# Performance work log

Hardware: AMD Instinct MI355X
Metric: run time of the kernel (lower is better)

## Reference

```python
import jax, jax.numpy as jnp
import numpy as np

N_NODES = 100000
N_EDGES = 1000000
DIM = 64


def setup_inputs() -> dict:
    key = jax.random.key(0)
    k1, k2, k3, k4 = jax.random.split(key, 4)
    node_emb = jax.random.normal(k1, (N_NODES, DIM), dtype=jnp.float32)
    rel_emb = jax.random.normal(k2, (N_EDGES, DIM), dtype=jnp.float32)
    src = jax.random.randint(k3, (N_EDGES,), 0, N_NODES, dtype=jnp.int64)
    dst = jax.random.randint(k4, (N_EDGES,), 0, N_NODES, dtype=jnp.int64)
    return {"node_emb": node_emb, "rel_emb": rel_emb, "src": src, "dst": dst}


def reference(node_emb, rel_emb, src, dst):
    # DistMult edge score: sum_d head[e,d] * rel[e,d] * tail[e,d]
    head = node_emb[src]          # (E, D) gather
    tail = node_emb[dst]          # (E, D) gather
    score = jnp.sum(head * rel_emb * tail, axis=-1)  # (E,)
    return score
```

## Files before the change

### kernel.cpp

```cpp
#include <hip/hip_runtime.h>
#include <hip/hip_bf16.h>


#define DIM 64
#define LANES_PER_EDGE 16

typedef __attribute__((ext_vector_type(4))) float  float4n;
typedef __attribute__((ext_vector_type(4))) unsigned short ushort4n;

__device__ __forceinline__ float bf2f(unsigned short u) {
    unsigned int x = ((unsigned int)u) << 16;
    return __builtin_bit_cast(float, x);
}

__device__ __forceinline__ unsigned short f2bf_rne(float f) {
    unsigned int x = __builtin_bit_cast(unsigned int, f);
    unsigned int lsb = (x >> 16) & 1u;
    x += 0x7fffu + lsb;
    return (unsigned short)(x >> 16);
}

__global__ __launch_bounds__(256) void convert_nodes_kernel(
    const float* __restrict__ node_emb,
    unsigned short* __restrict__ node_bf,
    int n_elems4)
{
    int i = blockIdx.x * blockDim.x + threadIdx.x;
    const int stride = gridDim.x * blockDim.x;
    for (; i < n_elems4; i += stride) {
        const float4n v = *reinterpret_cast<const float4n*>(node_emb + (size_t)i * 4);
        ushort4n o;
        o.x = f2bf_rne(v.x);
        o.y = f2bf_rne(v.y);
        o.z = f2bf_rne(v.z);
        o.w = f2bf_rne(v.w);
        *reinterpret_cast<ushort4n*>(node_bf + (size_t)i * 4) = o;
    }
}

__global__ __launch_bounds__(256) void distmult_score_bf16_kernel(
    const unsigned short* __restrict__ node_bf,
    const float* __restrict__ rel_emb,
    const int* __restrict__ src,
    const int* __restrict__ dst,
    float* __restrict__ out,
    int n_edges)
{
    const int tid   = blockIdx.x * blockDim.x + threadIdx.x;
    const int lane  = tid & (LANES_PER_EDGE - 1);
    const int group = tid >> 4;
    const int n_groups = (gridDim.x * blockDim.x) >> 4;
    const int off = lane * 4;

    for (int e = group; e < n_edges; e += 2 * n_groups) {
        const int e2 = e + n_groups;
        const bool has2 = (e2 < n_edges);

        const int s1 = src[e];
        const int d1 = dst[e];
        const int s2 = has2 ? src[e2] : 0;
        const int d2 = has2 ? dst[e2] : 0;

        const float4n  r1 = *reinterpret_cast<const float4n*>(rel_emb + (size_t)e * DIM + off);
        const ushort4n h1 = *reinterpret_cast<const ushort4n*>(node_bf + (size_t)s1 * DIM + off);
        const ushort4n t1 = *reinterpret_cast<const ushort4n*>(node_bf + (size_t)d1 * DIM + off);

        float4n  r2 = {0,0,0,0};
        ushort4n h2 = {0,0,0,0}, t2 = {0,0,0,0};
        if (has2) {
            r2 = *reinterpret_cast<const float4n*>(rel_emb + (size_t)e2 * DIM + off);
            h2 = *reinterpret_cast<const ushort4n*>(node_bf + (size_t)s2 * DIM + off);
            t2 = *reinterpret_cast<const ushort4n*>(node_bf + (size_t)d2 * DIM + off);
        }

        float p1 = bf2f(h1.x) * r1.x * bf2f(t1.x)
                 + bf2f(h1.y) * r1.y * bf2f(t1.y)
                 + bf2f(h1.z) * r1.z * bf2f(t1.z)
                 + bf2f(h1.w) * r1.w * bf2f(t1.w);

        p1 += __shfl_xor(p1, 1, 64);
        p1 += __shfl_xor(p1, 2, 64);
        p1 += __shfl_xor(p1, 4, 64);
        p1 += __shfl_xor(p1, 8, 64);
        if (lane == 0) out[e] = p1;

        if (has2) {
            float p2 = bf2f(h2.x) * r2.x * bf2f(t2.x)
                     + bf2f(h2.y) * r2.y * bf2f(t2.y)
                     + bf2f(h2.z) * r2.z * bf2f(t2.z)
                     + bf2f(h2.w) * r2.w * bf2f(t2.w);

            p2 += __shfl_xor(p2, 1, 64);
            p2 += __shfl_xor(p2, 2, 64);
            p2 += __shfl_xor(p2, 4, 64);
            p2 += __shfl_xor(p2, 8, 64);
            if (lane == 0) out[e2] = p2;
        }
    }
}

__global__ __launch_bounds__(256) void distmult_score_f32_kernel(
    const float* __restrict__ node_emb,
    const float* __restrict__ rel_emb,
    const int* __restrict__ src,
    const int* __restrict__ dst,
    float* __restrict__ out,
    int n_edges)
{
    const int tid   = blockIdx.x * blockDim.x + threadIdx.x;
    const int lane  = tid & (LANES_PER_EDGE - 1);
    const int group = tid >> 4;
    const int n_groups = (gridDim.x * blockDim.x) >> 4;
    const int off = lane * 4;

    for (int e = group; e < n_edges; e += n_groups) {
        const int s = src[e];
        const int d = dst[e];
        const float4n r = *reinterpret_cast<const float4n*>(rel_emb  + (size_t)e * DIM + off);
        const float4n h = *reinterpret_cast<const float4n*>(node_emb + (size_t)s * DIM + off);
        const float4n t = *reinterpret_cast<const float4n*>(node_emb + (size_t)d * DIM + off);

        float p = h.x * r.x * t.x + h.y * r.y * t.y + h.z * r.z * t.z + h.w * r.w * t.w;
        p += __shfl_xor(p, 1, 64);
        p += __shfl_xor(p, 2, 64);
        p += __shfl_xor(p, 4, 64);
        p += __shfl_xor(p, 8, 64);
        if (lane == 0) out[e] = p;
    }
}

extern "C" void kernel_launch(void* const* d_in, const int* in_sizes, int n_in,
                              void* d_out, int out_size, void* d_ws, size_t ws_size,
                              hipStream_t stream) {
    const float* node_emb = (const float*)d_in[0];
    const float* rel_emb  = (const float*)d_in[1];
    const int*   src      = (const int*)d_in[2];
    const int*   dst      = (const int*)d_in[3];
    float*       out      = (float*)d_out;

    const int n_edges     = in_sizes[2];
    const int n_node_elems = in_sizes[0];
    const size_t bf_bytes = (size_t)n_node_elems * sizeof(unsigned short);

    const int block = 256;
    long long blocks_needed = ((long long)n_edges * LANES_PER_EDGE + block - 1) / block;
    int grid = (int)(blocks_needed < 2048 ? blocks_needed : 2048);

    if (ws_size >= bf_bytes) {
        unsigned short* node_bf = (unsigned short*)d_ws;
        const int n4 = n_node_elems / 4;
        int cgrid = (n4 + block - 1) / block;
        if (cgrid > 2048) cgrid = 2048;
        convert_nodes_kernel<<<cgrid, block, 0, stream>>>(node_emb, node_bf, n4);
        distmult_score_bf16_kernel<<<grid, block, 0, stream>>>(node_bf, rel_emb, src, dst, out, n_edges);
    } else {
        distmult_score_f32_kernel<<<grid, block, 0, stream>>>(node_emb, rel_emb, src, dst, out, n_edges);
    }
}
```

Before: 85.84 us.

## Split scoring into two half-dimension passes to shrink gather working set

Splits the bf16 scoring kernel into two passes, each covering half of the embedding dimension. The intent is to halve the gathered node-table footprint per pass so it fits better in cache. The second pass reads back and accumulates into the output, and index and rel loads now use nontemporal hints. The cost is reading the src/dst indices twice, an extra output read-modify-write, and one more kernel launch.

```diff
diff --git a/kernel.cpp b/kernel.cpp
--- a/kernel.cpp
+++ b/kernel.cpp
@@ -3,7 +3,8 @@
 
 
 #define DIM 64
-#define LANES_PER_EDGE 16
+#define HALF_DIM 32
+#define LANES_PER_EDGE 8
 
 typedef __attribute__((ext_vector_type(4))) float  float4n;
 typedef __attribute__((ext_vector_type(4))) unsigned short ushort4n;
@@ -38,7 +39,8 @@
     }
 }
 
-__global__ __launch_bounds__(256) void distmult_score_bf16_kernel(
+template <int PASS>
+__global__ __launch_bounds__(256) void distmult_score_half_kernel(
     const unsigned short* __restrict__ node_bf,
     const float* __restrict__ rel_emb,
     const int* __restrict__ src,
@@ -48,53 +50,35 @@
 {
     const int tid   = blockIdx.x * blockDim.x + threadIdx.x;
     const int lane  = tid & (LANES_PER_EDGE - 1);
-    const int group = tid >> 4;
-    const int n_groups = (gridDim.x * blockDim.x) >> 4;
-    const int off = lane * 4;
+    const int group = tid >> 3;
+    const int n_groups = (gridDim.x * blockDim.x) >> 3;
+    const int off = PASS * HALF_DIM + lane * 4;
 
-    for (int e = group; e < n_edges; e += 2 * n_groups) {
-        const int e2 = e + n_groups;
-        const bool has2 = (e2 < n_edges);
+    for (int e = group; e < n_edges; e += n_groups) {
+        const int s = __builtin_nontemporal_load(src + e);
+        const int d = __builtin_nontemporal_load(dst + e);
 
-        const int s1 = src[e];
-        const int d1 = dst[e];
-        const int s2 = has2 ? src[e2] : 0;
-        const int d2 = has2 ? dst[e2] : 0;
+        const float4n  r = __builtin_nontemporal_load(
+            reinterpret_cast<const float4n*>(rel_emb + (size_t)e * DIM + off));
+        const ushort4n h = *reinterpret_cast<const ushort4n*>(node_bf + (size_t)s * DIM + off);
+        const ushort4n t = *reinterpret_cast<const ushort4n*>(node_bf + (size_t)d * DIM + off);
 
-        const float4n  r1 = *reinterpret_cast<const float4n*>(rel_emb + (size_t)e * DIM + off);
-        const ushort4n h1 = *reinterpret_cast<const ushort4n*>(node_bf + (size_t)s1 * DIM + off);
-        const ushort4n t1 = *reinterpret_cast<const ushort4n*>(node_bf + (size_t)d1 * DIM + off);
+        float p = bf2f(h.x) * r.x * bf2f(t.x)
+                + bf2f(h.y) * r.y * bf2f(t.y)
+                + bf2f(h.z) * r.z * bf2f(t.z)
+                + bf2f(h.w) * r.w * bf2f(t.w);
 
-        float4n  r2 = {0,0,0,0};
-        ushort4n h2 = {0,0,0,0}, t2 = {0,0,0,0};
-        if (has2) {
-            r2 = *reinterpret_cast<const float4n*>(rel_emb + (size_t)e2 * DIM + off);
-            h2 = *reinterpret_cast<const ushort4n*>(node_bf + (size_t)s2 * DIM + off);
-            t2 = *reinterpret_cast<const ushort4n*>(node_bf + (size_t)d2 * DIM + off);
-        }
+        p += __shfl_xor(p, 1, 64);
+        p += __shfl_xor(p, 2, 64);
+        p += __shfl_xor(p, 4, 64);
 
-        float p1 = bf2f(h1.x) * r1.x * bf2f(t1.x)
-                 + bf2f(h1.y) * r1.y * bf2f(t1.y)
-                 + bf2f(h1.z) * r1.z * bf2f(t1.z)
-                 + bf2f(h1.w) * r1.w * bf2f(t1.w);
-
-        p1 += __shfl_xor(p1, 1, 64);
-        p1 += __shfl_xor(p1, 2, 64);
-        p1 += __shfl_xor(p1, 4, 64);
-        p1 += __shfl_xor(p1, 8, 64);
-        if (lane == 0) out[e] = p1;
-
-        if (has2) {
-            float p2 = bf2f(h2.x) * r2.x * bf2f(t2.x)
-                     + bf2f(h2.y) * r2.y * bf2f(t2.y)
-                     + bf2f(h2.z) * r2.z * bf2f(t2.z)
-                     + bf2f(h2.w) * r2.w * bf2f(t2.w);
-
-            p2 += __shfl_xor(p2, 1, 64);
-            p2 += __shfl_xor(p2, 2, 64);
-            p2 += __shfl_xor(p2, 4, 64);
-            p2 += __shfl_xor(p2, 8, 64);
-            if (lane == 0) out[e2] = p2;
+        if (lane == 0) {
+            if (PASS == 0) {
+                __builtin_nontemporal_store(p, out + e);
+            } else {
+                const float prev = out[e];
+                __builtin_nontemporal_store(prev + p, out + e);
+            }
         }
     }
 }
@@ -108,7 +92,7 @@
     int n_edges)
 {
     const int tid   = blockIdx.x * blockDim.x + threadIdx.x;
-    const int lane  = tid & (LANES_PER_EDGE - 1);
+    const int lane  = tid & 15;
     const int group = tid >> 4;
     const int n_groups = (gridDim.x * blockDim.x) >> 4;
     const int off = lane * 4;
@@ -138,13 +122,11 @@
     const int*   dst      = (const int*)d_in[3];
     float*       out      = (float*)d_out;
 
-    const int n_edges     = in_sizes[2];
+    const int n_edges      = in_sizes[2];
     const int n_node_elems = in_sizes[0];
-    const size_t bf_bytes = (size_t)n_node_elems * sizeof(unsigned short);
+    const size_t bf_bytes  = (size_t)n_node_elems * sizeof(unsigned short);
 
     const int block = 256;
-    long long blocks_needed = ((long long)n_edges * LANES_PER_EDGE + block - 1) / block;
-    int grid = (int)(blocks_needed < 2048 ? blocks_needed : 2048);
 
     if (ws_size >= bf_bytes) {
         unsigned short* node_bf = (unsigned short*)d_ws;
@@ -152,8 +134,14 @@
         int cgrid = (n4 + block - 1) / block;
         if (cgrid > 2048) cgrid = 2048;
         convert_nodes_kernel<<<cgrid, block, 0, stream>>>(node_emb, node_bf, n4);
-        distmult_score_bf16_kernel<<<grid, block, 0, stream>>>(node_bf, rel_emb, src, dst, out, n_edges);
+
+        long long blocks_needed = ((long long)n_edges * LANES_PER_EDGE + block - 1) / block;
+        int grid = (int)(blocks_needed < 2048 ? blocks_needed : 2048);
+        distmult_score_half_kernel<0><<<grid, block, 0, stream>>>(node_bf, rel_emb, src, dst, out, n_edges);
+        distmult_score_half_kernel<1><<<grid, block, 0, stream>>>(node_bf, rel_emb, src, dst, out, n_edges);
     } else {
+        long long blocks_needed = ((long long)n_edges * 16 + block - 1) / block;
+        int grid = (int)(blocks_needed < 2048 ? blocks_needed : 2048);
         distmult_score_f32_kernel<<<grid, block, 0, stream>>>(node_emb, rel_emb, src, dst, out, n_edges);
     }
 }
```

New measurement: 111.1 us. 29.4% more time.
